# Kernel tuning notes

Measured on AMD Instinct MI355X. Metric: run time of the kernel, lower is better.

Reference implementation:

```python
import jax, jax.numpy as jnp
import numpy as np

N = 30000      # node_size / new_node_size
R = 1000       # rel_size
T = 300000     # triple_size (edges)
D = 128        # node_hid == rel_hid
B = 1024       # train pairs
NNZ = 600000   # nnz of ent_adj / rel_adj
DEPTH = 2
GAMMA = 3.0
EPS = 1e-12    # F.normalize eps


def setup_inputs():
    key = jax.random.key(0)
    ks = jax.random.split(key, 12)
    adj = jnp.stack([jax.random.randint(ks[0], (T,), 0, N),
                     jax.random.randint(ks[1], (T,), 0, N)]).astype(jnp.int64)
    # one relation per triple: row ids are 0..T-1, col ids are relation ids
    r_index = jnp.stack([jnp.arange(T),
                         jax.random.randint(ks[2], (T,), 0, R)]).astype(jnp.int64)
    r_val = jnp.ones((T,), jnp.float32)
    ent_adj = jnp.stack([jax.random.randint(ks[3], (NNZ,), 0, N),
                         jax.random.randint(ks[4], (NNZ,), 0, N)]).astype(jnp.int64)
    rel_adj = jnp.stack([jax.random.randint(ks[5], (NNZ,), 0, N),
                         jax.random.randint(ks[6], (NNZ,), 0, R)]).astype(jnp.int64)
    ent_emb = jax.random.normal(ks[7], (N, D), jnp.float32) * 0.05
    rel_emb = jax.random.normal(ks[8], (R, D), jnp.float32) * 0.05
    attn_e = jax.random.normal(ks[9], (DEPTH, D, 1), jnp.float32) * 0.1
    attn_r = jax.random.normal(ks[10], (DEPTH, D, 1), jnp.float32) * 0.1
    train_pairs = jax.random.randint(ks[11], (B, 2), 0, N).astype(jnp.int64)
    return dict(ent_emb=ent_emb, rel_emb=rel_emb, attn_e=attn_e, attn_r=attn_r,
                r_val=r_val, adj=adj, r_index=r_index, ent_adj=ent_adj,
                rel_adj=rel_adj, train_pairs=train_pairs)


def _segment_softmax(vals, seg, num):
    m = jax.ops.segment_max(vals, seg, num_segments=num)
    e = jnp.exp(vals - m[seg])
    s = jax.ops.segment_sum(e, seg, num_segments=num)
    return e / s[seg]


def _avg(adj, emb):
    # sparse softmax of an all-ones matrix over dim=1 == 1/deg per nonzero, then spmm
    row, col = adj[0], adj[1]
    deg = jax.ops.segment_sum(jnp.ones_like(row, emb.dtype), row, num_segments=N)
    return jax.ops.segment_sum(emb[col] / deg[row][:, None], row, num_segments=N)


def _gat(features, rel_emb, adj, r_index, r_val, kernels):
    features = jnp.tanh(features)
    outputs = [features]
    row, col = adj[0], adj[1]
    for l in range(DEPTH):
        # sparse [T,R] @ rel_emb  -> per-triple relation embedding
        tri_rel = jax.ops.segment_sum(r_val[:, None] * rel_emb[r_index[1]],
                                      r_index[0], num_segments=T)          # [T,D]
        tri_rel = tri_rel / jnp.maximum(
            jnp.linalg.norm(tri_rel, axis=1, keepdims=True), EPS)
        neighs = features[col]                                             # [T,D]
        neighs = neighs - 2.0 * jnp.sum(neighs * tri_rel, axis=1,
                                        keepdims=True) * tri_rel
        att = jnp.squeeze(tri_rel @ kernels[l], axis=-1)                   # [T]
        att = _segment_softmax(att, row, N)
        new_features = jax.ops.segment_sum(neighs * att[:, None], row,
                                           num_segments=N)
        features = jnp.tanh(new_features)
        outputs.append(features)
    return jnp.concatenate(outputs, axis=-1)  # [N, (DEPTH+1)*D]


def _align_loss(pairs, emb):
    l, r = pairs[:, 0], pairs[:, 1]
    l_emb, r_emb = emb[l], emb[r]
    pos = jnp.sum(jnp.square(l_emb - r_emb), axis=-1, keepdims=True)       # [B,1]

    def sqdist(A, Bm):
        return (jnp.sum(jnp.square(A), axis=1)[:, None]
                + jnp.sum(jnp.square(Bm), axis=1)[None, :]
                - 2.0 * A @ Bm.T)

    bi = jnp.arange(pairs.shape[0])
    mask = jnp.ones((pairs.shape[0], N), emb.dtype)
    mask = mask.at[bi, l].add(-1.0).at[bi, r].add(-1.0)  # 1 - onehot(l) - onehot(r)

    def norm_lse(loss):
        mu = jax.lax.stop_gradient(jnp.mean(loss, axis=-1, keepdims=True))
        sd = jax.lax.stop_gradient(jnp.std(loss, axis=-1, keepdims=True))
        loss = (loss - mu) / sd
        return jax.nn.logsumexp(20.0 * loss + 8.0, axis=-1)

    l_loss = norm_lse((pos - sqdist(l_emb, emb) + GAMMA) * mask)
    r_loss = norm_lse((pos - sqdist(r_emb, emb) + GAMMA) * mask)
    return jnp.mean(l_loss + r_loss)


def reference(ent_emb, rel_emb, attn_e, attn_r, r_val, adj, r_index,
              ent_adj, rel_adj, train_pairs):
    ent_feature = _avg(ent_adj, ent_emb)   # [N,D]
    rel_feature = _avg(rel_adj, rel_emb)   # [N,D]
    out_rel = _gat(rel_feature, rel_emb, adj, r_index, r_val, attn_r)
    out_ent = _gat(ent_feature, rel_emb, adj, r_index, r_val, attn_e)
    emb = jnp.concatenate([out_ent, out_rel], axis=-1)  # [N, 6*D]
    return _align_loss(train_pairs, emb)
```

## Files before the change

kernel.cpp:

```cpp
#include <hip/hip_runtime.h>
#include <math.h>

#define N_ENT 30000
#define R_REL 1000
#define T_EDGE 300000
#define B_PAIR 1024
#define NNZ_E 600000
#define GAMMAF 3.0f
#define EPSV 1e-12f
#define EMBD 768
#define NPAD 30720
#define NT128 240
#define PTILES 480

typedef _Float16 half8 __attribute__((ext_vector_type(8)));
typedef _Float16 half4v __attribute__((ext_vector_type(4)));
typedef _Float16 half2v __attribute__((ext_vector_type(2)));
typedef float f32x4 __attribute__((ext_vector_type(4)));

__device__ inline void gl_lds16(const _Float16* g, _Float16* l){
  __builtin_amdgcn_global_load_lds(
      (const __attribute__((address_space(1))) unsigned int*)g,
      (__attribute__((address_space(3))) unsigned int*)l, 16, 0, 0);
}

__device__ inline float waveRedSum(float v){
  #pragma unroll
  for(int m=32;m>=1;m>>=1) v += __shfl_xor(v, m, 64);
  return v;
}

__device__ inline float fast_tanh(float x){
  x = fminf(10.f, fmaxf(-10.f, x));
  float e = __expf(2.f*x);
  return (e-1.f)/(e+1.f);
}

__global__ __launch_bounds__(256) void k_count3(const int* __restrict__ rA, int* cA,
                                                const int* __restrict__ rE, int* cE,
                                                const int* __restrict__ rR, int* cR){
  int e = blockIdx.x*256 + threadIdx.x;
  if(e < T_EDGE) atomicAdd(&cA[rA[e]], 1);
  if(e < NNZ_E){ atomicAdd(&cE[rE[e]], 1); atomicAdd(&cR[rR[e]], 1); }
}

__global__ __launch_bounds__(1024) void k_scan3(const int* c0, int* s0, int* u0,
                                                const int* c1, int* s1, int* u1,
                                                const int* c2, int* s2, int* u2){
  const int* cnt = blockIdx.x==0 ? c0 : (blockIdx.x==1 ? c1 : c2);
  int* start     = blockIdx.x==0 ? s0 : (blockIdx.x==1 ? s1 : s2);
  int* cursor    = blockIdx.x==0 ? u0 : (blockIdx.x==1 ? u1 : u2);
  __shared__ int wsum[16];
  __shared__ int carry;
  int tid = threadIdx.x, lane = tid & 63, wid = tid >> 6;
  if(tid==0) carry = 0;
  __syncthreads();
  for(int base=0; base<N_ENT; base+=1024){
    int i = base + tid;
    int v = (i<N_ENT)? cnt[i] : 0;
    int x = v;
    #pragma unroll
    for(int off=1; off<64; off<<=1){ int t=__shfl_up(x,off,64); if(lane>=off) x+=t; }
    if(lane==63) wsum[wid]=x;
    __syncthreads();
    if(wid==0){
      int s = (lane<16)? wsum[lane] : 0;
      #pragma unroll
      for(int off=1; off<16; off<<=1){ int t=__shfl_up(s,off,64); if(lane>=off) s+=t; }
      if(lane<16) wsum[lane]=s;
    }
    __syncthreads();
    int wexcl = (wid==0)? 0 : wsum[wid-1];
    int excl = carry + wexcl + x - v;
    if(i<N_ENT){ start[i]=excl; cursor[i]=excl; }
    int tot = wsum[15];
    __syncthreads();
    if(tid==0) carry += tot;
    __syncthreads();
  }
  if(tid==0) start[N_ENT] = carry;
}

__global__ __launch_bounds__(256) void k_scatter3(
      const int* __restrict__ rA, const int* __restrict__ cAj, const int* __restrict__ rid,
      int* uA, int* scolA, int* sridA,
      const int* __restrict__ rE, const int* __restrict__ cEj, int* uE, int* scolE,
      const int* __restrict__ rR, const int* __restrict__ cRj, int* uR, int* scolR){
  int e = blockIdx.x*256 + threadIdx.x;
  if(e < T_EDGE){
    int p = atomicAdd(&uA[rA[e]], 1);
    scolA[p] = cAj[e];
    sridA[p] = rid[e];
  }
  if(e < NNZ_E){
    int p = atomicAdd(&uE[rE[e]], 1);
    scolE[p] = cEj[e];
    int q = atomicAdd(&uR[rR[e]], 1);
    scolR[q] = cRj[e];
  }
}

__global__ __launch_bounds__(256) void k_prep(const float* __restrict__ ent, const float* __restrict__ rel,
      const float* __restrict__ ae, const float* __restrict__ ar,
      _Float16* ehE, _Float16* ehR, _Float16* Eh, _Float16* relnH, float* expdot){
  int i = blockIdx.x*256 + threadIdx.x;
  if(i < N_ENT*128) ehE[i] = (_Float16)ent[i];
  if(i < R_REL*128) ehR[i] = (_Float16)rel[i];
  if(i < (NPAD-N_ENT)*EMBD) Eh[(size_t)N_ENT*EMBD + i] = (_Float16)0.f;
  int r = i >> 6;
  if(r < R_REL){
    int lane = i & 63;
    float2 v = *(const float2*)(rel + (size_t)r*128 + lane*2);
    float ss = waveRedSum(v.x*v.x + v.y*v.y);
    float nrm = fmaxf(sqrtf(ss), EPSV);
    float2 u; u.x = v.x/nrm; u.y = v.y/nrm;
    half2v uh = {(_Float16)u.x, (_Float16)u.y};
    *(half2v*)(relnH + (size_t)r*128 + lane*2) = uh;
    const float* ks[4] = {ae, ae+128, ar, ar+128};
    #pragma unroll
    for(int k=0;k<4;k++){
      float2 w = *(const float2*)(ks[k] + lane*2);
      float d = waveRedSum(u.x*w.x + u.y*w.y);
      if(lane==0) expdot[k*R_REL + r] = __expf(d);
    }
  }
}

__global__ __launch_bounds__(256) void k_avg2(const int* __restrict__ startE, const int* __restrict__ scolE,
                        const _Float16* __restrict__ srcE,
                        const int* __restrict__ startR, const int* __restrict__ scolR,
                        const _Float16* __restrict__ srcR,
                        _Float16* featC, _Float16* Eh){
  int which = blockIdx.y;
  const int* start = which? startR : startE;
  const int* scol  = which? scolR : scolE;
  const _Float16* src = which? srcR : srcE;
  int pairOff = which? 2 : 0;
  int coloff  = which? 384 : 0;
  int r = blockIdx.x*4 + (threadIdx.x>>6);
  int lane = threadIdx.x & 63;
  int s0 = start[r], s1 = start[r+1];
  float ax=0.f, ay=0.f;
  int e = s0;
  for(; e+1<s1; e+=2){
    int c0 = scol[e], c1 = scol[e+1];
    half2v v0 = *(const half2v*)(src + (size_t)c0*128 + lane*2);
    half2v v1 = *(const half2v*)(src + (size_t)c1*128 + lane*2);
    ax += (float)v0[0] + (float)v1[0]; ay += (float)v0[1] + (float)v1[1];
  }
  if(e<s1){
    int c0 = scol[e];
    half2v v0 = *(const half2v*)(src + (size_t)c0*128 + lane*2);
    ax += (float)v0[0]; ay += (float)v0[1];
  }
  float inv = (s1>s0) ? 1.0f/(float)(s1-s0) : 0.f;
  float vx = fast_tanh(ax*inv), vy = fast_tanh(ay*inv);
  half2v hv = {(_Float16)vx, (_Float16)vy};
  *(half2v*)(featC + (size_t)r*256 + lane*4 + pairOff) = hv;
  *(half2v*)(Eh + (size_t)r*EMBD + coloff + lane*2) = hv;
}

__global__ __launch_bounds__(256) void k_edge2(const int* __restrict__ start, const int* __restrict__ scol,
      const int* __restrict__ srid, const _Float16* __restrict__ relnH,
      const float* __restrict__ expE, const float* __restrict__ expR,
      const _Float16* __restrict__ featIn, _Float16* featOut, _Float16* Eh, int colEnt, int colRel){
  int r = blockIdx.x*4 + (threadIdx.x>>6);
  int lane = threadIdx.x & 63;
  int s0 = start[r], s1 = start[r+1];
  float aEx=0,aEy=0,aRx=0,aRy=0, swE=0, swR=0;
  int e = s0;
  for(; e+1<s1; e+=2){
    int c0=scol[e], q0=srid[e], c1=scol[e+1], q1=srid[e+1];
    float wE0=expE[q0], wR0=expR[q0], wE1=expE[q1], wR1=expR[q1];
    half2v u0h = *(const half2v*)(relnH + (size_t)q0*128 + lane*2);
    half2v u1h = *(const half2v*)(relnH + (size_t)q1*128 + lane*2);
    half4v h0 = *(const half4v*)(featIn + (size_t)c0*256 + lane*4);
    half4v h1 = *(const half4v*)(featIn + (size_t)c1*256 + lane*4);
    float u0x=(float)u0h[0], u0y=(float)u0h[1], u1x=(float)u1h[0], u1y=(float)u1h[1];
    float e0x=(float)h0[0], e0y=(float)h0[1], r0x=(float)h0[2], r0y=(float)h0[3];
    float e1x=(float)h1[0], e1y=(float)h1[1], r1x=(float)h1[2], r1y=(float)h1[3];
    float d0 = e0x*u0x + e0y*u0y;
    float d1 = r0x*u0x + r0y*u0y;
    float d2 = e1x*u1x + e1y*u1y;
    float d3 = r1x*u1x + r1y*u1y;
    #pragma unroll
    for(int m=32;m>=1;m>>=1){
      d0 += __shfl_xor(d0,m,64); d1 += __shfl_xor(d1,m,64);
      d2 += __shfl_xor(d2,m,64); d3 += __shfl_xor(d3,m,64);
    }
    aEx += wE0*(e0x - 2.f*d0*u0x) + wE1*(e1x - 2.f*d2*u1x);
    aEy += wE0*(e0y - 2.f*d0*u0y) + wE1*(e1y - 2.f*d2*u1y);
    aRx += wR0*(r0x - 2.f*d1*u0x) + wR1*(r1x - 2.f*d3*u1x);
    aRy += wR0*(r0y - 2.f*d1*u0y) + wR1*(r1y - 2.f*d3*u1y);
    swE += wE0+wE1; swR += wR0+wR1;
  }
  if(e<s1){
    int c0=scol[e], q0=srid[e];
    float wE0=expE[q0], wR0=expR[q0];
    half2v u0h = *(const half2v*)(relnH + (size_t)q0*128 + lane*2);
    half4v h0 = *(const half4v*)(featIn + (size_t)c0*256 + lane*4);
    float u0x=(float)u0h[0], u0y=(float)u0h[1];
    float e0x=(float)h0[0], e0y=(float)h0[1], r0x=(float)h0[2], r0y=(float)h0[3];
    float d0 = e0x*u0x + e0y*u0y;
    float d1 = r0x*u0x + r0y*u0y;
    #pragma unroll
    for(int m=32;m>=1;m>>=1){ d0 += __shfl_xor(d0,m,64); d1 += __shfl_xor(d1,m,64); }
    aEx += wE0*(e0x - 2.f*d0*u0x);
    aEy += wE0*(e0y - 2.f*d0*u0y);
    aRx += wR0*(r0x - 2.f*d1*u0x);
    aRy += wR0*(r0y - 2.f*d1*u0y);
    swE += wE0; swR += wR0;
  }
  float iE = (s1>s0) ? 1.f/swE : 0.f;
  float iR = (s1>s0) ? 1.f/swR : 0.f;
  float vEx = fast_tanh(aEx*iE), vEy = fast_tanh(aEy*iE);
  float vRx = fast_tanh(aRx*iR), vRy = fast_tanh(aRy*iR);
  half4v ov = {(_Float16)vEx,(_Float16)vEy,(_Float16)vRx,(_Float16)vRy};
  *(half4v*)(featOut + (size_t)r*256 + lane*4) = ov;
  half2v he = {(_Float16)vEx,(_Float16)vEy};
  half2v hr = {(_Float16)vRx,(_Float16)vRy};
  *(half2v*)(Eh + (size_t)r*EMBD + colEnt + lane*2) = he;
  *(half2v*)(Eh + (size_t)r*EMBD + colRel + lane*2) = hr;
}

__global__ __launch_bounds__(256) void k_gather(const _Float16* __restrict__ Eh, const int* __restrict__ tp,
                         _Float16* Wh, float* cvec){
  int i = blockIdx.x; int tid = threadIdx.x;
  int l = tp[2*i], r = tp[2*i+1];
  float sl=0.f, sr=0.f, sp=0.f;
  for(int c=tid;c<EMBD;c+=256){
    _Float16 lh = Eh[(size_t)l*EMBD+c], rh = Eh[(size_t)r*EMBD+c];
    float le = (float)lh, re = (float)rh;
    Wh[(size_t)i*EMBD+c]=lh; Wh[(size_t)(B_PAIR+i)*EMBD+c]=rh;
    sl += le*le; sr += re*re; float d = le-re; sp += d*d;
  }
  __shared__ float s0[256], s1[256], s2[256];
  s0[tid]=sl; s1[tid]=sr; s2[tid]=sp;
  __syncthreads();
  for(int w=128;w>0;w>>=1){
    if(tid<w){ s0[tid]+=s0[tid+w]; s1[tid]+=s1[tid+w]; s2[tid]+=s2[tid+w]; }
    __syncthreads();
  }
  if(tid==0){
    float pos = s2[0];
    cvec[i]        = pos + GAMMAF - s0[0];
    cvec[B_PAIR+i] = pos + GAMMAF - s1[0];
  }
}

__global__ __launch_bounds__(256) void k_qnstats(const _Float16* __restrict__ Eh, float* qn,
                           float* Svec, float* Pvec, float* QQ){
  int wid = threadIdx.x>>6, lane = threadIdx.x&63;
  int gw = blockIdx.x*4 + wid;
  float s[12], p[12];
  #pragma unroll
  for(int q=0;q<12;q++){ s[q]=0.f; p[q]=0.f; }
  float q1=0.f, q2=0.f;
  for(int r=gw; r<NPAD; r+=960){
    if(r >= N_ENT){ if(lane==0) qn[r] = 1e30f; continue; }
    float v[12]; float ss=0.f;
    #pragma unroll
    for(int q=0;q<12;q++){ v[q] = (float)Eh[(size_t)r*EMBD + lane + 64*q]; ss += v[q]*v[q]; }
    ss = waveRedSum(ss);
    if(lane==0){ qn[r] = ss; q1 += ss; q2 += ss*ss; }
    #pragma unroll
    for(int q=0;q<12;q++){ s[q] += v[q]; p[q] += ss*v[q]; }
  }
  #pragma unroll
  for(int q=0;q<12;q++){
    unsafeAtomicAdd(&Svec[lane + 64*q], s[q]);
    unsafeAtomicAdd(&Pvec[lane + 64*q], p[q]);
  }
  if(lane==0){ unsafeAtomicAdd(&QQ[0], q1); unsafeAtomicAdd(&QQ[1], q2); }
}

__global__ __launch_bounds__(256) void k_transp(const _Float16* __restrict__ Eh, _Float16* embT){
  __shared__ __align__(16) _Float16 til[64][72];
  int r0 = blockIdx.x*64, c0 = blockIdx.y*64;
  int t = threadIdx.x;
  int rr = t>>3, c8 = (t&7)*8;
  #pragma unroll
  for(int p=0;p<2;p++){
    int gr = r0 + rr + p*32;
    uint4 v = make_uint4(0u,0u,0u,0u);
    if(gr < N_ENT) v = *(const uint4*)(Eh + (size_t)gr*EMBD + c0 + c8);
    *(uint4*)&til[rr + p*32][c8] = v;
  }
  __syncthreads();
  #pragma unroll
  for(int p=0;p<2;p++){
    int cc = rr + p*32;
    __align__(16) _Float16 tmp[8];
    #pragma unroll
    for(int j=0;j<8;j++) tmp[j] = til[c8 + j][cc];
    *(uint4*)(embT + (size_t)(c0+cc)*NPAD + r0 + c8) = *(uint4*)tmp;
  }
}

__global__ __launch_bounds__(256) void k_syrk(const _Float16* __restrict__ embT, float* G){
  __shared__ __align__(16) _Float16 As[128*64];
  __shared__ __align__(16) _Float16 Bs[128*64];
  int tid = threadIdx.x;
  int w = tid>>6, lane = tid&63;
  int quad = lane>>4, l15 = lane&15;
  int lr = lane>>3, lc = lane&7;
  int wm = (w>>1)*64, wn = (w&1)*64;
  int m0 = blockIdx.y*128, n0 = blockIdx.x*128;
  int kbeg = blockIdx.z*3840;
  int kend = kbeg + 3840; if(kend > NPAD) kend = NPAD;
  f32x4 acc[4][4];
  #pragma unroll
  for(int i=0;i<4;i++)
    #pragma unroll
    for(int j=0;j<4;j++) acc[i][j] = (f32x4){0.f,0.f,0.f,0.f};
  for(int k0=kbeg;k0<kend;k0+=64){
    #pragma unroll
    for(int p=0;p<4;p++){
      int r = p*32 + w*8 + lr;
      int cg = lc ^ (r&7);
      gl_lds16(embT + (size_t)(m0+r)*NPAD + k0 + cg*8, As + (p*32 + w*8)*64);
      gl_lds16(embT + (size_t)(n0+r)*NPAD + k0 + cg*8, Bs + (p*32 + w*8)*64);
    }
    __syncthreads();
    #pragma unroll
    for(int ks=0;ks<2;ks++){
      half8 af[4], bf[4];
      #pragma unroll
      for(int i=0;i<4;i++){
        int ml = wm + i*16 + l15;
        af[i] = *(half8*)(As + ml*64 + (((ks<<2)|quad) ^ (ml&7))*8);
      }
      #pragma unroll
      for(int j=0;j<4;j++){
        int nl = wn + j*16 + l15;
        bf[j] = *(half8*)(Bs + nl*64 + (((ks<<2)|quad) ^ (nl&7))*8);
      }
      #pragma unroll
      for(int i=0;i<4;i++)
        #pragma unroll
        for(int j=0;j<4;j++)
          acc[i][j] = __builtin_amdgcn_mfma_f32_16x16x32_f16(af[i], bf[j], acc[i][j], 0,0,0);
    }
    __syncthreads();
  }
  #pragma unroll
  for(int i=0;i<4;i++){
    #pragma unroll
    for(int r=0;r<4;r++){
      int m = m0 + wm + i*16 + quad*4 + r;
      #pragma unroll
      for(int j=0;j<4;j++){
        int n = n0 + wn + j*16 + l15;
        unsafeAtomicAdd(&G[(size_t)m*EMBD + n], acc[i][j][r]);
      }
    }
  }
}

__global__ __launch_bounds__(256) void k_gemmTh(const _Float16* __restrict__ Wh, const float* __restrict__ G,
                                                float* Tm){
  int tid = threadIdx.x, w = tid>>6, lane = tid&63;
  int quad = lane>>4, l15 = lane&15;
  int n0 = blockIdx.x*64;
  #pragma unroll
  for(int half=0; half<2; half++){
    int m0 = (blockIdx.y*8 + half*4 + w)*64;
    f32x4 acc[4][4];
    #pragma unroll
    for(int i=0;i<4;i++)
      #pragma unroll
      for(int j=0;j<4;j++) acc[i][j] = (f32x4){0.f,0.f,0.f,0.f};
    const _Float16* aB[4]; const float* bB[4];
    #pragma unroll
    for(int i=0;i<4;i++){
      aB[i] = Wh + (size_t)(m0+i*16+l15)*EMBD + quad*8;
      bB[i] = G  + (size_t)(n0+i*16+l15)*EMBD + quad*8;
    }
    for(int ks=0; ks<24; ks++){
      half8 af[4], bf[4];
      #pragma unroll
      for(int i=0;i<4;i++) af[i] = *(const half8*)(aB[i] + ks*32);
      #pragma unroll
      for(int j=0;j<4;j++){
        float4 f0 = *(const float4*)(bB[j] + ks*32);
        float4 f1 = *(const float4*)(bB[j] + ks*32 + 4);
        half8 h = {(_Float16)f0.x,(_Float16)f0.y,(_Float16)f0.z,(_Float16)f0.w,
                   (_Float16)f1.x,(_Float16)f1.y,(_Float16)f1.z,(_Float16)f1.w};
        bf[j] = h;
      }
      #pragma unroll
      for(int i=0;i<4;i++)
        #pragma unroll
        for(int j=0;j<4;j++)
          acc[i][j] = __builtin_amdgcn_mfma_f32_16x16x32_f16(af[i], bf[j], acc[i][j], 0,0,0);
    }
    #pragma unroll
    for(int i=0;i<4;i++)
      #pragma unroll
      for(int r=0;r<4;r++){
        int mg = m0 + i*16 + quad*4 + r;
        #pragma unroll
        for(int j=0;j<4;j++)
          Tm[(size_t)mg*EMBD + n0 + j*16 + l15] = acc[i][j][r];
      }
  }
}

__global__ __launch_bounds__(256) void k_rowstats(const _Float16* __restrict__ Wh, const float* __restrict__ Tm,
      const _Float16* __restrict__ Eh, const float* __restrict__ qn, const float* __restrict__ cvec,
      const int* __restrict__ tp, const float* __restrict__ Svec, const float* __restrict__ Pvec,
      const float* __restrict__ QQ, float* alpha, float* betav){
  int row = blockIdx.x*4 + (threadIdx.x>>6);
  int lane = threadIdx.x & 63;
  if(row >= 2*B_PAIR) return;
  int pi = row & (B_PAIR-1);
  int lp = tp[2*pi], rp = tp[2*pi+1];
  float d1=0,d2=0,d3=0,dl=0,dr=0;
  #pragma unroll
  for(int k=0;k<12;k++){
    int d = lane + 64*k;
    float a = (float)Wh[(size_t)row*EMBD + d];
    d1 += a*Svec[d];
    d2 += a*Pvec[d];
    d3 += a*Tm[(size_t)row*EMBD + d];
    dl += a*(float)Eh[(size_t)lp*EMBD + d];
    dr += a*(float)Eh[(size_t)rp*EMBD + d];
  }
  d1=waveRedSum(d1); d2=waveRedSum(d2); d3=waveRedSum(d3);
  dl=waveRedSum(dl); dr=waveRedSum(dr);
  if(lane==0){
    double c = (double)cvec[row], Q = (double)QQ[0], Q2 = (double)QQ[1], Nn = (double)N_ENT;
    double su  = Nn*c - Q + 2.0*(double)d1;
    double su2 = Nn*c*c - 2.0*c*Q + Q2 + 4.0*(c*(double)d1 - (double)d2) + 4.0*(double)d3;
    double ul = c - (double)qn[lp] + 2.0*(double)dl;
    double ur = c - (double)qn[rp] + 2.0*(double)dr;
    su -= ul + ur;
    if(lp != rp) su2 -= ul*ul + ur*ur;
    double mu = su/Nn;
    double var = su2/Nn - mu*mu;
    double sd = sqrt(fmax(var, 0.0));
    double al = 20.0/sd;
    alpha[row] = (float)al;
    betav[row] = (float)(8.0 - al*mu);
  }
}

__device__ inline void lseMerge(float& mx, float& sm, float om, float os){
  if(om > mx){ sm = sm*expf(mx-om) + os; mx = om; }
  else if(om != -INFINITY){ sm += os*expf(om-mx); }
}

__global__ __launch_bounds__(256,3) void k_gemmB(const _Float16* __restrict__ Wh, const _Float16* __restrict__ Eh,
    const float* __restrict__ cvec, const float* __restrict__ qn, const int* __restrict__ tp,
    const float* __restrict__ alpha, const float* __restrict__ betav, float* pm, float* ps){
  __shared__ __align__(16) _Float16 As[128*64];
  __shared__ __align__(16) _Float16 Bs[128*64];
  int id = blockIdx.x;
  int ntile = (id & 7) + ((id >> 7) << 3);
  int m0 = ((id >> 3) & 15) * 128;
  int n0 = ntile * 128;
  int tid = threadIdx.x;
  int w = tid>>6, lane = tid&63;
  int quad = lane>>4, l15 = lane&15;
  int lr = lane>>3, lc = lane&7;
  int wm = (w&1)*64, wn = (w>>1)*64;
  f32x4 acc[4][4];
  #pragma unroll
  for(int i=0;i<4;i++)
    #pragma unroll
    for(int j=0;j<4;j++) acc[i][j] = (f32x4){0.f,0.f,0.f,0.f};
  for(int k0=0;k0<EMBD;k0+=64){
    #pragma unroll
    for(int p=0;p<4;p++){
      int r = p*32 + w*8 + lr;
      int cg = lc ^ (r&7);
      gl_lds16(Wh + (size_t)(m0+r)*EMBD + k0 + cg*8, As + (p*32 + w*8)*64);
      gl_lds16(Eh + (size_t)(n0+r)*EMBD + k0 + cg*8, Bs + (p*32 + w*8)*64);
    }
    __syncthreads();
    #pragma unroll
    for(int ks=0;ks<2;ks++){
      half8 af[4], bf[4];
      #pragma unroll
      for(int i=0;i<4;i++){
        int ml = wm + i*16 + l15;
        af[i] = *(half8*)(As + ml*64 + (((ks<<2)|quad) ^ (ml&7))*8);
      }
      #pragma unroll
      for(int j=0;j<4;j++){
        int nl = wn + j*16 + l15;
        bf[j] = *(half8*)(Bs + nl*64 + (((ks<<2)|quad) ^ (nl&7))*8);
      }
      #pragma unroll
      for(int i=0;i<4;i++)
        #pragma unroll
        for(int j=0;j<4;j++)
          acc[i][j] = __builtin_amdgcn_mfma_f32_16x16x32_f16(af[i], bf[j], acc[i][j], 0,0,0);
    }
    __syncthreads();
  }
  float qv[4]; int jv[4];
  #pragma unroll
  for(int j=0;j<4;j++){ jv[j] = n0 + wn + j*16 + l15; qv[j] = qn[jv[j]]; }
  int ptile = ntile*2 + (w>>1);
  #pragma unroll
  for(int i=0;i<4;i++){
    int mbase = m0 + wm + i*16 + quad*4;
    #pragma unroll
    for(int r=0;r<4;r++){
      int mg = mbase + r;
      int pi = mg & (B_PAIR-1);
      int lp = tp[2*pi], rp = tp[2*pi+1];
      float cv = cvec[mg], al = alpha[mg], be = betav[mg];
      float mx = -INFINITY, sm = 0.f;
      #pragma unroll
      for(int j=0;j<4;j++){
        float u = fmaf(2.f, acc[i][j][r], cv - qv[j]);
        float z = fmaf(al, u, be);
        if(jv[j]==lp || jv[j]==rp) z = (lp==rp) ? fmaf(-al, u, be) : be;
        if(z > mx){ sm = sm*__expf(mx - z) + 1.f; mx = z; }
        else sm += __expf(z - mx);
      }
      #pragma unroll
      for(int m=8;m>=1;m>>=1){
        float om = __shfl_xor(mx, m, 64), os = __shfl_xor(sm, m, 64);
        lseMerge(mx, sm, om, os);
      }
      if(l15==0){ pm[(size_t)mg*PTILES + ptile] = mx; ps[(size_t)mg*PTILES + ptile] = sm; }
    }
  }
}

__global__ __launch_bounds__(256) void k_lse2(const float* __restrict__ pm, const float* __restrict__ ps,
                        float* accum, int* done, float* out){
  __shared__ float shm[256], shs[256];
  int row = blockIdx.x, tid = threadIdx.x;
  float mx = -INFINITY, sm = 0.f;
  for(int t=tid;t<PTILES;t+=256) lseMerge(mx, sm, pm[(size_t)row*PTILES+t], ps[(size_t)row*PTILES+t]);
  shm[tid]=mx; shs[tid]=sm;
  __syncthreads();
  for(int w=128;w>0;w>>=1){
    if(tid<w){
      float m2=shm[tid], s2=shs[tid];
      lseMerge(m2, s2, shm[tid+w], shs[tid+w]);
      shm[tid]=m2; shs[tid]=s2;
    }
    __syncthreads();
  }
  if(tid==0){
    float l = shm[0] + logf(shs[0]);
    atomicAdd(accum, l);
    __threadfence();
    int t = atomicAdd(done, 1);
    if(t == 2*B_PAIR - 1){
      __threadfence();
      float total = atomicAdd(accum, 0.0f);
      out[0] = total / (float)B_PAIR;
    }
  }
}

extern "C" void kernel_launch(void* const* d_in, const int* in_sizes, int n_in,
                              void* d_out, int out_size, void* d_ws, size_t ws_size,
                              hipStream_t stream) {
  const float* ent_emb = (const float*)d_in[0];
  const float* rel_emb = (const float*)d_in[1];
  const float* attn_e  = (const float*)d_in[2];
  const float* attn_r  = (const float*)d_in[3];
  const int* adj     = (const int*)d_in[5];
  const int* r_index = (const int*)d_in[6];
  const int* ent_adj = (const int*)d_in[7];
  const int* rel_adj = (const int*)d_in[8];
  const int* tp      = (const int*)d_in[9];
  float* out = (float*)d_out;

  const int* adj_row = adj;
  const int* adj_col = adj + T_EDGE;
  const int* rid1    = r_index + T_EDGE;

  char* base = (char*)d_ws;
  size_t off = 0;
  auto A = [&](size_t b)->void*{ void* p = base + off; off = (off + b + 255) & ~(size_t)255; return p; };
  int*   cntA  = (int*)  A((size_t)N_ENT*4);
  int*   cntE  = (int*)  A((size_t)N_ENT*4);
  int*   cntR  = (int*)  A((size_t)N_ENT*4);
  float* G     = (float*)A((size_t)EMBD*EMBD*4);
  float* Svec  = (float*)A(EMBD*4);
  float* Pvec  = (float*)A(EMBD*4);
  float* QQ    = (float*)A(2*4);
  float* accum = (float*)A(4);
  int*   done  = (int*)  A(4);
  size_t zero_end = off;
  int* startA = (int*)A((size_t)(N_ENT+1)*4);
  int* startE = (int*)A((size_t)(N_ENT+1)*4);
  int* startR = (int*)A((size_t)(N_ENT+1)*4);
  int* curA   = (int*)A((size_t)N_ENT*4);
  int* curE   = (int*)A((size_t)N_ENT*4);
  int* curR   = (int*)A((size_t)N_ENT*4);
  int* scolA  = (int*)A((size_t)T_EDGE*4);
  int* sridA  = (int*)A((size_t)T_EDGE*4);
  int* scolE  = (int*)A((size_t)NNZ_E*4);
  int* scolR  = (int*)A((size_t)NNZ_E*4);
  _Float16* Eh = (_Float16*)A((size_t)NPAD*EMBD*2);
  char* X = (char*)A((size_t)EMBD*NPAD*2);
  _Float16* featC0 = (_Float16*)X;
  _Float16* featC1 = (_Float16*)(X + 16u*1024u*1024u);
  _Float16* embT   = (_Float16*)X;
  float*    pm     = (float*)X;
  float*    ps     = (float*)(X + 8u*1024u*1024u);
  _Float16* relnH  = (_Float16*)A((size_t)R_REL*128*2);
  _Float16* ehE   = (_Float16*)A((size_t)N_ENT*128*2);
  _Float16* ehR   = (_Float16*)A((size_t)R_REL*128*2);
  float* expdot  = (float*)A(4*R_REL*4);
  _Float16* Wh   = (_Float16*)A((size_t)2*B_PAIR*EMBD*2);
  float* Tm      = (float*)A((size_t)2*B_PAIR*EMBD*4);
  float* cvec    = (float*)A(2*B_PAIR*4);
  float* qn      = (float*)A((size_t)NPAD*4);
  float* alpha   = (float*)A(2*B_PAIR*4);
  float* betav   = (float*)A(2*B_PAIR*4);
  (void)ws_size; (void)in_sizes; (void)n_in; (void)out_size;

  hipMemsetAsync(d_ws, 0, zero_end, stream);

  k_count3<<<(NNZ_E+255)/256, 256, 0, stream>>>(adj_row, cntA, ent_adj, cntE, rel_adj, cntR);
  k_scan3<<<3, 1024, 0, stream>>>(cntA, startA, curA, cntE, startE, curE, cntR, startR, curR);
  k_scatter3<<<(NNZ_E+255)/256, 256, 0, stream>>>(adj_row, adj_col, rid1, curA, scolA, sridA,
                                                  ent_adj, ent_adj+NNZ_E, curE, scolE,
                                                  rel_adj, rel_adj+NNZ_E, curR, scolR);

  k_prep<<<(N_ENT*128+255)/256, 256, 0, stream>>>(ent_emb, rel_emb, attn_e, attn_r,
                                                  ehE, ehR, Eh, relnH, expdot);

  dim3 gavg(N_ENT/4, 2);
  k_avg2<<<gavg, 256, 0, stream>>>(startE, scolE, ehE, startR, scolR, ehR, featC0, Eh);
  k_edge2<<<N_ENT/4, 256, 0, stream>>>(startA, scolA, sridA, relnH, expdot + 0*R_REL, expdot + 2*R_REL,
                                       featC0, featC1, Eh, 128, 512);
  k_edge2<<<N_ENT/4, 256, 0, stream>>>(startA, scolA, sridA, relnH, expdot + 1*R_REL, expdot + 3*R_REL,
                                       featC1, featC0, Eh, 256, 640);

  k_gather<<<B_PAIR, 256, 0, stream>>>(Eh, tp, Wh, cvec);
  k_qnstats<<<240, 256, 0, stream>>>(Eh, qn, Svec, Pvec, QQ);
  dim3 gtr(NPAD/64, 12);
  k_transp<<<gtr, 256, 0, stream>>>(Eh, embT);
  dim3 gsy(6, 6, 8);
  k_syrk<<<gsy, 256, 0, stream>>>(embT, G);
  dim3 gT(EMBD/64, 4);
  k_gemmTh<<<gT, 256, 0, stream>>>(Wh, G, Tm);
  k_rowstats<<<2*B_PAIR/4, 256, 0, stream>>>(Wh, Tm, Eh, qn, cvec, tp, Svec, Pvec, QQ, alpha, betav);
  k_gemmB<<<NT128*16, 256, 0, stream>>>(Wh, Eh, cvec, qn, tp, alpha, betav, pm, ps);
  k_lse2<<<2*B_PAIR, 256, 0, stream>>>(pm, ps, accum, done, out);
}
```

Before: 889.4 us.

## Parallelize CSR scan, merge count into prep, fuse post kernels, rebalance syrk

Replaces the single-block-per-array serial scan with a three-phase multi-block scan (block scan, partial scan, offset add), and folds edge counting into the prep kernel. Merges gather, transpose and norm-statistics kernels into one launch selected by block index. Reworks syrk to 576 blocks with smaller K slices mapped across XCDs. The aim is fewer serialized launches and more parallelism in latency-bound setup phases, at the cost of extra launches for the scan and more atomics in the atomic-contended prep kernel.

```diff
diff --git a/kernel.cpp b/kernel.cpp
--- a/kernel.cpp
+++ b/kernel.cpp
@@ -12,6 +12,7 @@
 #define NPAD 30720
 #define NT128 240
 #define PTILES 480
+#define SCB 118
 
 typedef _Float16 half8 __attribute__((ext_vector_type(8)));
 typedef _Float16 half4v __attribute__((ext_vector_type(4)));
@@ -36,49 +37,86 @@
   return (e-1.f)/(e+1.f);
 }
 
-__global__ __launch_bounds__(256) void k_count3(const int* __restrict__ rA, int* cA,
-                                                const int* __restrict__ rE, int* cE,
-                                                const int* __restrict__ rR, int* cR){
-  int e = blockIdx.x*256 + threadIdx.x;
-  if(e < T_EDGE) atomicAdd(&cA[rA[e]], 1);
-  if(e < NNZ_E){ atomicAdd(&cE[rE[e]], 1); atomicAdd(&cR[rR[e]], 1); }
-}
-
-__global__ __launch_bounds__(1024) void k_scan3(const int* c0, int* s0, int* u0,
-                                                const int* c1, int* s1, int* u1,
-                                                const int* c2, int* s2, int* u2){
-  const int* cnt = blockIdx.x==0 ? c0 : (blockIdx.x==1 ? c1 : c2);
-  int* start     = blockIdx.x==0 ? s0 : (blockIdx.x==1 ? s1 : s2);
-  int* cursor    = blockIdx.x==0 ? u0 : (blockIdx.x==1 ? u1 : u2);
-  __shared__ int wsum[16];
-  __shared__ int carry;
-  int tid = threadIdx.x, lane = tid & 63, wid = tid >> 6;
-  if(tid==0) carry = 0;
+__global__ __launch_bounds__(256) void k_prep(const float* __restrict__ ent, const float* __restrict__ rel,
+      const float* __restrict__ ae, const float* __restrict__ ar,
+      _Float16* ehE, _Float16* ehR, _Float16* Eh, _Float16* relnH, float* expdot,
+      const int* __restrict__ rA, int* cA, const int* __restrict__ rE, int* cE,
+      const int* __restrict__ rR, int* cR){
+  int i = blockIdx.x*256 + threadIdx.x;
+  if(i < N_ENT*128) ehE[i] = (_Float16)ent[i];
+  if(i < R_REL*128) ehR[i] = (_Float16)rel[i];
+  if(i < (NPAD-N_ENT)*EMBD) Eh[(size_t)N_ENT*EMBD + i] = (_Float16)0.f;
+  if(i < T_EDGE) atomicAdd(&cA[rA[i]], 1);
+  if(i < NNZ_E){ atomicAdd(&cE[rE[i]], 1); atomicAdd(&cR[rR[i]], 1); }
+  int r = i >> 6;
+  if(r < R_REL){
+    int lane = i & 63;
+    float2 v = *(const float2*)(rel + (size_t)r*128 + lane*2);
+    float ss = waveRedSum(v.x*v.x + v.y*v.y);
+    float nrm = fmaxf(sqrtf(ss), EPSV);
+    float2 u; u.x = v.x/nrm; u.y = v.y/nrm;
+    half2v uh = {(_Float16)u.x, (_Float16)u.y};
+    *(half2v*)(relnH + (size_t)r*128 + lane*2) = uh;
+    const float* ks[4] = {ae, ae+128, ar, ar+128};
+    #pragma unroll
+    for(int k=0;k<4;k++){
+      float2 w = *(const float2*)(ks[k] + lane*2);
+      float d = waveRedSum(u.x*w.x + u.y*w.y);
+      if(lane==0) expdot[k*R_REL + r] = __expf(d);
+    }
+  }
+}
+
+__global__ __launch_bounds__(256) void k_scanA(const int* c0, const int* c1, const int* c2,
+                                               int* s0, int* s1, int* s2, int* part){
+  const int* cnt = blockIdx.y==0 ? c0 : (blockIdx.y==1 ? c1 : c2);
+  int* start     = blockIdx.y==0 ? s0 : (blockIdx.y==1 ? s1 : s2);
+  __shared__ int wsum[4];
+  int i = blockIdx.x*256 + threadIdx.x;
+  int lane = threadIdx.x & 63, wid = threadIdx.x >> 6;
+  int v = (i < N_ENT) ? cnt[i] : 0;
+  int x = v;
+  #pragma unroll
+  for(int off=1; off<64; off<<=1){ int t=__shfl_up(x,off,64); if(lane>=off) x+=t; }
+  if(lane==63) wsum[wid] = x;
   __syncthreads();
-  for(int base=0; base<N_ENT; base+=1024){
-    int i = base + tid;
-    int v = (i<N_ENT)? cnt[i] : 0;
-    int x = v;
-    #pragma unroll
-    for(int off=1; off<64; off<<=1){ int t=__shfl_up(x,off,64); if(lane>=off) x+=t; }
-    if(lane==63) wsum[wid]=x;
-    __syncthreads();
-    if(wid==0){
-      int s = (lane<16)? wsum[lane] : 0;
-      #pragma unroll
-      for(int off=1; off<16; off<<=1){ int t=__shfl_up(s,off,64); if(lane>=off) s+=t; }
-      if(lane<16) wsum[lane]=s;
-    }
-    __syncthreads();
-    int wexcl = (wid==0)? 0 : wsum[wid-1];
-    int excl = carry + wexcl + x - v;
-    if(i<N_ENT){ start[i]=excl; cursor[i]=excl; }
-    int tot = wsum[15];
-    __syncthreads();
-    if(tid==0) carry += tot;
-    __syncthreads();
-  }
-  if(tid==0) start[N_ENT] = carry;
+  int woff = 0;
+  #pragma unroll
+  for(int k=0;k<3;k++) if(k < wid) woff += wsum[k];
+  if(i < N_ENT) start[i] = woff + x - v;
+  if(threadIdx.x == 255) part[blockIdx.y*SCB + blockIdx.x] = woff + x;
+}
+
+__global__ __launch_bounds__(256) void k_scanB(int* part, int* tots){
+  int wid = threadIdx.x>>6, lane = threadIdx.x&63;
+  if(wid >= 3) return;
+  int base = wid*SCB;
+  int v0 = part[base + lane];
+  int i1 = 64 + lane;
+  int v1 = (i1 < SCB) ? part[base + i1] : 0;
+  int x0 = v0, x1 = v1;
+  #pragma unroll
+  for(int off=1; off<64; off<<=1){
+    int t0=__shfl_up(x0,off,64), t1=__shfl_up(x1,off,64);
+    if(lane>=off){ x0+=t0; x1+=t1; }
+  }
+  int t0 = __shfl(x0, 63, 64);
+  int t1 = __shfl(x1, 63, 64);
+  part[base + lane] = x0 - v0;
+  if(i1 < SCB) part[base + i1] = t0 + x1 - v1;
+  if(lane == 0) tots[wid] = t0 + t1;
+}
+
+__global__ __launch_bounds__(256) void k_scanC(int* s0, int* s1, int* s2,
+                                               int* u0, int* u1, int* u2,
+                                               const int* part, const int* tots){
+  int y = blockIdx.y;
+  int* start  = y==0 ? s0 : (y==1 ? s1 : s2);
+  int* cursor = y==0 ? u0 : (y==1 ? u1 : u2);
+  int i = blockIdx.x*256 + threadIdx.x;
+  int off = part[y*SCB + blockIdx.x];
+  if(i < N_ENT){ int v = start[i] + off; start[i] = v; cursor[i] = v; }
+  if(i == 0) start[N_ENT] = tots[y];
 }
 
 __global__ __launch_bounds__(256) void k_scatter3(
@@ -97,32 +135,6 @@
     scolE[p] = cEj[e];
     int q = atomicAdd(&uR[rR[e]], 1);
     scolR[q] = cRj[e];
-  }
-}
-
-__global__ __launch_bounds__(256) void k_prep(const float* __restrict__ ent, const float* __restrict__ rel,
-      const float* __restrict__ ae, const float* __restrict__ ar,
-      _Float16* ehE, _Float16* ehR, _Float16* Eh, _Float16* relnH, float* expdot){
-  int i = blockIdx.x*256 + threadIdx.x;
-  if(i < N_ENT*128) ehE[i] = (_Float16)ent[i];
-  if(i < R_REL*128) ehR[i] = (_Float16)rel[i];
-  if(i < (NPAD-N_ENT)*EMBD) Eh[(size_t)N_ENT*EMBD + i] = (_Float16)0.f;
-  int r = i >> 6;
-  if(r < R_REL){
-    int lane = i & 63;
-    float2 v = *(const float2*)(rel + (size_t)r*128 + lane*2);
-    float ss = waveRedSum(v.x*v.x + v.y*v.y);
-    float nrm = fmaxf(sqrtf(ss), EPSV);
-    float2 u; u.x = v.x/nrm; u.y = v.y/nrm;
-    half2v uh = {(_Float16)u.x, (_Float16)u.y};
-    *(half2v*)(relnH + (size_t)r*128 + lane*2) = uh;
-    const float* ks[4] = {ae, ae+128, ar, ar+128};
-    #pragma unroll
-    for(int k=0;k<4;k++){
-      float2 w = *(const float2*)(ks[k] + lane*2);
-      float d = waveRedSum(u.x*w.x + u.y*w.y);
-      if(lane==0) expdot[k*R_REL + r] = __expf(d);
-    }
   }
 }
 
@@ -223,91 +235,94 @@
   *(half2v*)(Eh + (size_t)r*EMBD + colRel + lane*2) = hr;
 }
 
-__global__ __launch_bounds__(256) void k_gather(const _Float16* __restrict__ Eh, const int* __restrict__ tp,
-                         _Float16* Wh, float* cvec){
-  int i = blockIdx.x; int tid = threadIdx.x;
-  int l = tp[2*i], r = tp[2*i+1];
-  float sl=0.f, sr=0.f, sp=0.f;
-  for(int c=tid;c<EMBD;c+=256){
-    _Float16 lh = Eh[(size_t)l*EMBD+c], rh = Eh[(size_t)r*EMBD+c];
-    float le = (float)lh, re = (float)rh;
-    Wh[(size_t)i*EMBD+c]=lh; Wh[(size_t)(B_PAIR+i)*EMBD+c]=rh;
-    sl += le*le; sr += re*re; float d = le-re; sp += d*d;
-  }
-  __shared__ float s0[256], s1[256], s2[256];
-  s0[tid]=sl; s1[tid]=sr; s2[tid]=sp;
-  __syncthreads();
-  for(int w=128;w>0;w>>=1){
-    if(tid<w){ s0[tid]+=s0[tid+w]; s1[tid]+=s1[tid+w]; s2[tid]+=s2[tid+w]; }
+__global__ __launch_bounds__(256) void k_post(const _Float16* __restrict__ Eh, _Float16* embT,
+      const int* __restrict__ tp, _Float16* Wh, float* cvec,
+      float* qn, float* Svec, float* Pvec, float* QQ){
+  __shared__ __align__(16) _Float16 til[64][72];
+  __shared__ float sh0[256], sh1[256], sh2[256];
+  int b = blockIdx.x;
+  int tid = threadIdx.x;
+  if(b < 5760){
+    int r0 = (b % 480)*64, c0 = (b / 480)*64;
+    int rr = tid>>3, c8 = (tid&7)*8;
+    #pragma unroll
+    for(int p=0;p<2;p++){
+      int gr = r0 + rr + p*32;
+      uint4 v = make_uint4(0u,0u,0u,0u);
+      if(gr < N_ENT) v = *(const uint4*)(Eh + (size_t)gr*EMBD + c0 + c8);
+      *(uint4*)&til[rr + p*32][c8] = v;
+    }
     __syncthreads();
-  }
-  if(tid==0){
-    float pos = s2[0];
-    cvec[i]        = pos + GAMMAF - s0[0];
-    cvec[B_PAIR+i] = pos + GAMMAF - s1[0];
-  }
-}
-
-__global__ __launch_bounds__(256) void k_qnstats(const _Float16* __restrict__ Eh, float* qn,
-                           float* Svec, float* Pvec, float* QQ){
-  int wid = threadIdx.x>>6, lane = threadIdx.x&63;
-  int gw = blockIdx.x*4 + wid;
-  float s[12], p[12];
-  #pragma unroll
-  for(int q=0;q<12;q++){ s[q]=0.f; p[q]=0.f; }
-  float q1=0.f, q2=0.f;
-  for(int r=gw; r<NPAD; r+=960){
-    if(r >= N_ENT){ if(lane==0) qn[r] = 1e30f; continue; }
-    float v[12]; float ss=0.f;
-    #pragma unroll
-    for(int q=0;q<12;q++){ v[q] = (float)Eh[(size_t)r*EMBD + lane + 64*q]; ss += v[q]*v[q]; }
-    ss = waveRedSum(ss);
-    if(lane==0){ qn[r] = ss; q1 += ss; q2 += ss*ss; }
-    #pragma unroll
-    for(int q=0;q<12;q++){ s[q] += v[q]; p[q] += ss*v[q]; }
-  }
-  #pragma unroll
-  for(int q=0;q<12;q++){
-    unsafeAtomicAdd(&Svec[lane + 64*q], s[q]);
-    unsafeAtomicAdd(&Pvec[lane + 64*q], p[q]);
-  }
-  if(lane==0){ unsafeAtomicAdd(&QQ[0], q1); unsafeAtomicAdd(&QQ[1], q2); }
-}
-
-__global__ __launch_bounds__(256) void k_transp(const _Float16* __restrict__ Eh, _Float16* embT){
-  __shared__ __align__(16) _Float16 til[64][72];
-  int r0 = blockIdx.x*64, c0 = blockIdx.y*64;
-  int t = threadIdx.x;
-  int rr = t>>3, c8 = (t&7)*8;
-  #pragma unroll
-  for(int p=0;p<2;p++){
-    int gr = r0 + rr + p*32;
-    uint4 v = make_uint4(0u,0u,0u,0u);
-    if(gr < N_ENT) v = *(const uint4*)(Eh + (size_t)gr*EMBD + c0 + c8);
-    *(uint4*)&til[rr + p*32][c8] = v;
-  }
-  __syncthreads();
-  #pragma unroll
-  for(int p=0;p<2;p++){
-    int cc = rr + p*32;
-    __align__(16) _Float16 tmp[8];
-    #pragma unroll
-    for(int j=0;j<8;j++) tmp[j] = til[c8 + j][cc];
-    *(uint4*)(embT + (size_t)(c0+cc)*NPAD + r0 + c8) = *(uint4*)tmp;
+    #pragma unroll
+    for(int p=0;p<2;p++){
+      int cc = rr + p*32;
+      __align__(16) _Float16 tmp[8];
+      #pragma unroll
+      for(int j=0;j<8;j++) tmp[j] = til[c8 + j][cc];
+      *(uint4*)(embT + (size_t)(c0+cc)*NPAD + r0 + c8) = *(uint4*)tmp;
+    }
+  } else if(b < 5760 + B_PAIR){
+    int i = b - 5760;
+    int l = tp[2*i], r = tp[2*i+1];
+    float sl=0.f, sr=0.f, sp=0.f;
+    for(int c=tid;c<EMBD;c+=256){
+      _Float16 lh = Eh[(size_t)l*EMBD+c], rh = Eh[(size_t)r*EMBD+c];
+      float le = (float)lh, re = (float)rh;
+      Wh[(size_t)i*EMBD+c]=lh; Wh[(size_t)(B_PAIR+i)*EMBD+c]=rh;
+      sl += le*le; sr += re*re; float d = le-re; sp += d*d;
+    }
+    sh0[tid]=sl; sh1[tid]=sr; sh2[tid]=sp;
+    __syncthreads();
+    for(int w=128;w>0;w>>=1){
+      if(tid<w){ sh0[tid]+=sh0[tid+w]; sh1[tid]+=sh1[tid+w]; sh2[tid]+=sh2[tid+w]; }
+      __syncthreads();
+    }
+    if(tid==0){
+      float pos = sh2[0];
+      cvec[i]        = pos + GAMMAF - sh0[0];
+      cvec[B_PAIR+i] = pos + GAMMAF - sh1[0];
+    }
+  } else {
+    int wid = tid>>6, lane = tid&63;
+    int gw = (b - 5760 - B_PAIR)*4 + wid;
+    float s[12], p[12];
+    #pragma unroll
+    for(int q=0;q<12;q++){ s[q]=0.f; p[q]=0.f; }
+    float q1=0.f, q2=0.f;
+    for(int r=gw; r<NPAD; r+=960){
+      if(r >= N_ENT){ if(lane==0) qn[r] = 1e30f; continue; }
+      float v[12]; float ss=0.f;
+      #pragma unroll
+      for(int q=0;q<12;q++){ v[q] = (float)Eh[(size_t)r*EMBD + lane + 64*q]; ss += v[q]*v[q]; }
+      ss = waveRedSum(ss);
+      ss = __shfl(ss, 0, 64);
+      if(lane==0){ qn[r] = ss; q1 += ss; q2 += ss*ss; }
+      #pragma unroll
+      for(int q=0;q<12;q++){ s[q] += v[q]; p[q] += ss*v[q]; }
+    }
+    #pragma unroll
+    for(int q=0;q<12;q++){
+      unsafeAtomicAdd(&Svec[lane + 64*q], s[q]);
+      unsafeAtomicAdd(&Pvec[lane + 64*q], p[q]);
+    }
+    if(lane==0){ unsafeAtomicAdd(&QQ[0], q1); unsafeAtomicAdd(&QQ[1], q2); }
   }
 }
 
 __global__ __launch_bounds__(256) void k_syrk(const _Float16* __restrict__ embT, float* G){
   __shared__ __align__(16) _Float16 As[128*64];
   __shared__ __align__(16) _Float16 Bs[128*64];
+  int id = blockIdx.x;
+  int xcd = id & 7, rest = id >> 3;
+  int kslc = xcd + 8*(rest/36);
+  int tile = rest % 36;
+  int m0 = (tile/6)*128, n0 = (tile%6)*128;
+  int kbeg = kslc*1920, kend = kbeg + 1920;
   int tid = threadIdx.x;
   int w = tid>>6, lane = tid&63;
   int quad = lane>>4, l15 = lane&15;
   int lr = lane>>3, lc = lane&7;
   int wm = (w>>1)*64, wn = (w&1)*64;
-  int m0 = blockIdx.y*128, n0 = blockIdx.x*128;
-  int kbeg = blockIdx.z*3840;
-  int kend = kbeg + 3840; if(kend > NPAD) kend = NPAD;
   f32x4 acc[4][4];
   #pragma unroll
   for(int i=0;i<4;i++)
@@ -597,6 +612,8 @@
   int* curA   = (int*)A((size_t)N_ENT*4);
   int* curE   = (int*)A((size_t)N_ENT*4);
   int* curR   = (int*)A((size_t)N_ENT*4);
+  int* part   = (int*)A(3*SCB*4);
+  int* tots   = (int*)A(3*4);
   int* scolA  = (int*)A((size_t)T_EDGE*4);
   int* sridA  = (int*)A((size_t)T_EDGE*4);
   int* scolE  = (int*)A((size_t)NNZ_E*4);
@@ -622,14 +639,17 @@
 
   hipMemsetAsync(d_ws, 0, zero_end, stream);
 
-  k_count3<<<(NNZ_E+255)/256, 256, 0, stream>>>(adj_row, cntA, ent_adj, cntE, rel_adj, cntR);
-  k_scan3<<<3, 1024, 0, stream>>>(cntA, startA, curA, cntE, startE, curE, cntR, startR, curR);
+  k_prep<<<(N_ENT*128+255)/256, 256, 0, stream>>>(ent_emb, rel_emb, attn_e, attn_r,
+                                                  ehE, ehR, Eh, relnH, expdot,
+                                                  adj_row, cntA, ent_adj, cntE, rel_adj, cntR);
+
+  dim3 gsa(SCB, 3);
+  k_scanA<<<gsa, 256, 0, stream>>>(cntA, cntE, cntR, startA, startE, startR, part);
+  k_scanB<<<1, 256, 0, stream>>>(part, tots);
+  k_scanC<<<gsa, 256, 0, stream>>>(startA, startE, startR, curA, curE, curR, part, tots);
   k_scatter3<<<(NNZ_E+255)/256, 256, 0, stream>>>(adj_row, adj_col, rid1, curA, scolA, sridA,
                                                   ent_adj, ent_adj+NNZ_E, curE, scolE,
                                                   rel_adj, rel_adj+NNZ_E, curR, scolR);
-
-  k_prep<<<(N_ENT*128+255)/256, 256, 0, stream>>>(ent_emb, rel_emb, attn_e, attn_r,
-                                                  ehE, ehR, Eh, relnH, expdot);
 
   dim3 gavg(N_ENT/4, 2);
   k_avg2<<<gavg, 256, 0, stream>>>(startE, scolE, ehE, startR, scolR, ehR, featC0, Eh);
@@ -638,12 +658,9 @@
   k_edge2<<<N_ENT/4, 256, 0, stream>>>(startA, scolA, sridA, relnH, expdot + 1*R_REL, expdot + 3*R_REL,
                                        featC1, featC0, Eh, 256, 640);
 
-  k_gather<<<B_PAIR, 256, 0, stream>>>(Eh, tp, Wh, cvec);
-  k_qnstats<<<240, 256, 0, stream>>>(Eh, qn, Svec, Pvec, QQ);
-  dim3 gtr(NPAD/64, 12);
-  k_transp<<<gtr, 256, 0, stream>>>(Eh, embT);
-  dim3 gsy(6, 6, 8);
-  k_syrk<<<gsy, 256, 0, stream>>>(embT, G);
+  k_post<<<5760 + B_PAIR + 240, 256, 0, stream>>>(Eh, embT, tp, Wh, cvec, qn, Svec, Pvec, QQ);
+
+  k_syrk<<<576, 256, 0, stream>>>(embT, G);
   dim3 gT(EMBD/64, 4);
   k_gemmTh<<<gT, 256, 0, stream>>>(Wh, G, Tm);
   k_rowstats<<<2*B_PAIR/4, 256, 0, stream>>>(Wh, Tm, Eh, qn, cvec, tp, Svec, Pvec, QQ, alpha, betav);
```

New measurement: 881.0 us. About the same (-0.9%).
